# Kernel optimization log

Measured on AMD Instinct MI355X. Metric: run time of the kernel, lower is better.

Reference implementation:

```python
import jax, jax.numpy as jnp
import numpy as np

N = 12000   # num_node
D = 128     # hiddenSize
HID = 256   # hidden_channels
B = 512     # batch
L = 20      # citing history length
F = 400     # title_vec + journal_vec
FF = 512    # transformer dim_feedforward
NH = 4      # heads
STDV = float(1.0 / np.sqrt(D))


def _unif(k, shape):
    return jax.random.uniform(k, shape, jnp.float32, -STDV, STDV)


def setup_inputs():
    key = jax.random.key(0)
    ks = jax.random.split(key, 40)
    inp = {}
    inp['embedding'] = _unif(ks[0], (N, D))
    inp['f1_w'] = _unif(ks[1], (D, F)); inp['f1_b'] = _unif(ks[2], (D,))
    # two GNN modules, each a 2-layer GCN (assumed structure)
    inp['gcn0_w1'] = _unif(ks[3], (D, HID)); inp['gcn0_b1'] = _unif(ks[4], (HID,))
    inp['gcn0_w2'] = _unif(ks[5], (HID, D)); inp['gcn0_b2'] = _unif(ks[6], (D,))
    inp['gcn1_w1'] = _unif(ks[7], (D, HID)); inp['gcn1_b1'] = _unif(ks[8], (HID,))
    inp['gcn1_w2'] = _unif(ks[9], (HID, D)); inp['gcn1_b2'] = _unif(ks[10], (D,))
    # transformer encoder layer (post-norm, relu), reset_parameters makes ALL weights uniform
    inp['in_proj_w'] = _unif(ks[11], (3 * D, D)); inp['in_proj_b'] = _unif(ks[12], (3 * D,))
    inp['out_proj_w'] = _unif(ks[13], (D, D)); inp['out_proj_b'] = _unif(ks[14], (D,))
    inp['ln1_s'] = _unif(ks[15], (D,)); inp['ln1_b'] = _unif(ks[16], (D,))
    inp['ff1_w'] = _unif(ks[17], (FF, D)); inp['ff1_b'] = _unif(ks[18], (FF,))
    inp['ff2_w'] = _unif(ks[19], (D, FF)); inp['ff2_b'] = _unif(ks[20], (D,))
    inp['ln2_s'] = _unif(ks[21], (D,)); inp['ln2_b'] = _unif(ks[22], (D,))
    # forward inputs
    inp['adj_mat'] = jax.random.uniform(ks[23], (N, N), jnp.float32) * (2.0 / N)  # ~row-stochastic
    inp['node_feature'] = jax.random.normal(ks[24], (N, F), jnp.float32)
    inp['H_content'] = jax.random.normal(ks[25], (B, 10), jnp.float32)  # unused in forward
    inp['citing'] = jax.random.randint(ks[26], (B,), 0, N)
    inp['h_items'] = jax.random.randint(ks[27], (B,), 0, N)  # unused in forward
    inp['u_seqs'] = jax.random.randint(ks[28], (B, L), 0, N)
    inp['u_seqs_num'] = jax.random.randint(ks[29], (B,), 1, L)  # unused in forward
    return inp


def _layer_norm(x, s, b):
    m = x.mean(-1, keepdims=True)
    v = ((x - m) ** 2).mean(-1, keepdims=True)
    return (x - m) * jax.lax.rsqrt(v + 1e-5) * s + b


def reference(embedding, f1_w, f1_b,
              gcn0_w1, gcn0_b1, gcn0_w2, gcn0_b2,
              gcn1_w1, gcn1_b1, gcn1_w2, gcn1_b2,
              in_proj_w, in_proj_b, out_proj_w, out_proj_b,
              ln1_s, ln1_b, ff1_w, ff1_b, ff2_w, ff2_b, ln2_s, ln2_b,
              adj_mat, node_feature, H_content,
              citing, h_items, u_seqs, u_seqs_num):
    # embedding gate
    nf = node_feature @ f1_w.T + f1_b          # [N, D]
    x = embedding * nf                          # [N, D]
    # GCN stack: each GNN = relu((A x) W1 + b1) -> (A h) W2 + b2
    for (w1, b1, w2, b2) in ((gcn0_w1, gcn0_b1, gcn0_w2, gcn0_b2),
                             (gcn1_w1, gcn1_b1, gcn1_w2, gcn1_b2)):
        h = jax.nn.relu((adj_mat @ x) @ w1 + b1)
        x = (adj_mat @ h) @ w2 + b2
    item = x                                    # [N, D]
    seq = item[u_seqs]                          # [B, L, D]
    # torch TransformerEncoderLayer with batch_first=False: dim0 (B) is the
    # sequence axis, dim1 (L) is the batch axis (faithful to original code).
    qkv = seq @ in_proj_w.T + in_proj_b         # [B, L, 3D]
    q, k, v = jnp.split(qkv, 3, axis=-1)
    dh = D // NH
    q = q.reshape(B, L, NH, dh) * (1.0 / np.sqrt(dh))
    k = k.reshape(B, L, NH, dh)
    v = v.reshape(B, L, NH, dh)
    att = jax.nn.softmax(jnp.einsum('snhd,tnhd->nhst', q, k), axis=-1)  # attn over seq axis s,t=B
    o = jnp.einsum('nhst,tnhd->snhd', att, v).reshape(B, L, D)
    o = o @ out_proj_w.T + out_proj_b
    x1 = _layer_norm(seq + o, ln1_s, ln1_b)
    ff = jax.nn.relu(x1 @ ff1_w.T + ff1_b) @ ff2_w.T + ff2_b
    x2 = _layer_norm(x1 + ff, ln2_s, ln2_b)
    citing_vec = x2.mean(axis=1)                # mean over dim=1 (L), [B, D]
    citing_feats = nf[citing]                   # [B, D]
    citing_paper = jnp.concatenate([citing_vec, citing_feats], axis=1)  # [B, 2D]
    cited_paper = jnp.concatenate([item, nf], axis=1)                   # [N, 2D]
    scores = citing_paper @ cited_paper.T       # [B, N]
    return scores
```

## Files before the change

### kernel.cpp

```cpp
#include <hip/hip_runtime.h>
#include <hip/hip_bf16.h>

typedef __hip_bfloat16 bf;
typedef __attribute__((ext_vector_type(4))) float f32x4;
typedef __attribute__((ext_vector_type(8))) __bf16 bf16x8;
typedef __attribute__((ext_vector_type(8))) short short8;

#define NN 12000
#define DD 128
#define HIDC 256
#define BBATCH 512
#define LSEQ 20
#define FFEAT 400
#define FFDIM 512
#define KSLICE 2400

__device__ __forceinline__ float b2f(bf v) { return __bfloat162float(v); }
__device__ __forceinline__ bf f2b(float v) { return __float2bfloat16(v); }
__device__ __forceinline__ float us2f(unsigned short u) {
    return __uint_as_float(((unsigned int)u) << 16);
}
__device__ __forceinline__ unsigned short f2us(float f) {
    bf h = __float2bfloat16(f);
    return __builtin_bit_cast(unsigned short, h);
}

__device__ __forceinline__ void gload_lds16(const bf* g, bf* l) {
    __builtin_amdgcn_global_load_lds(
        (__attribute__((address_space(1))) void*)(g),
        (__attribute__((address_space(3))) void*)(l),
        16, 0, 0);
}

template<bool F32>
__device__ __forceinline__ short8 ld8(const void* p, long long idx) {
    if (F32) {
        const float* fp = (const float*)p + idx;
        f32x4 u0 = *(const f32x4*)fp;
        f32x4 u1 = *(const f32x4*)(fp + 4);
        short8 s;
        s[0] = (short)f2us(u0[0]); s[1] = (short)f2us(u0[1]);
        s[2] = (short)f2us(u0[2]); s[3] = (short)f2us(u0[3]);
        s[4] = (short)f2us(u1[0]); s[5] = (short)f2us(u1[1]);
        s[6] = (short)f2us(u1[2]); s[7] = (short)f2us(u1[3]);
        return s;
    } else {
        return *(const short8*)((const bf*)p + idx);
    }
}

template<bool F32>
__device__ __forceinline__ bf ldelem(const void* p, long long idx) {
    if (F32) return f2b(((const float*)p)[idx]);
    return ((const bf*)p)[idx];
}

__global__ __launch_bounds__(256) void adj_gemm(
    const bf* __restrict__ A,
    const bf* __restrict__ Bt,
    float* __restrict__ part)
{
    alignas(16) __shared__ bf As[128 * 32];
    alignas(16) __shared__ bf Bs[128 * 32];
    const int tid = threadIdx.x;
    const int lane = tid & 63;
    const int w = tid >> 6;
    const int z = blockIdx.y;
    const long long k0 = (long long)z * KSLICE;
    int m0 = blockIdx.x * 128;
    if (m0 > NN - 128) m0 = NN - 128;

    const int r0 = 16 * (2 * w)     + (lane >> 2);
    const int r1 = 16 * (2 * w + 1) + (lane >> 2);
    const int cp = lane & 3;
    const int cl0 = cp ^ ((r0 >> 1) & 3);
    const int cl1 = cp ^ ((r1 >> 1) & 3);
    const bf* ga0 = A + (long long)(m0 + r0) * NN + k0 + cl0 * 8;
    const bf* ga1 = A + (long long)(m0 + r1) * NN + k0 + cl1 * 8;
    const bf* gb0 = Bt + (long long)r0 * NN + k0 + cl0 * 8;
    const bf* gb1 = Bt + (long long)r1 * NN + k0 + cl1 * 8;
    bf* lA0 = &As[16 * (2 * w) * 32];
    bf* lA1 = &As[16 * (2 * w + 1) * 32];
    bf* lB0 = &Bs[16 * (2 * w) * 32];
    bf* lB1 = &Bs[16 * (2 * w + 1) * 32];

    const int wr = (w >> 1) * 64, wc = (w & 1) * 64;
    const int fr = lane & 15;
    const int cphys = (lane >> 4) ^ ((fr >> 1) & 3);
    f32x4 acc[4][4] = {};

    for (int ks = 0; ks < KSLICE; ks += 32) {
        gload_lds16(ga0, lA0);
        gload_lds16(ga1, lA1);
        gload_lds16(gb0, lB0);
        gload_lds16(gb1, lB1);
        ga0 += 32; ga1 += 32; gb0 += 32; gb1 += 32;
        __syncthreads();
        bf16x8 af[4], bfr[4];
        #pragma unroll
        for (int i = 0; i < 4; i++)
            af[i] = *(const bf16x8*)((const char*)As + (wr + i * 16 + fr) * 64 + cphys * 16);
        #pragma unroll
        for (int i = 0; i < 4; i++)
            bfr[i] = *(const bf16x8*)((const char*)Bs + (wc + i * 16 + fr) * 64 + cphys * 16);
        #pragma unroll
        for (int mi = 0; mi < 4; mi++)
            #pragma unroll
            for (int ni = 0; ni < 4; ni++)
                acc[mi][ni] = __builtin_amdgcn_mfma_f32_16x16x32_bf16(
                    af[mi], bfr[ni], acc[mi][ni], 0, 0, 0);
        __syncthreads();
    }

    float* C = part + (long long)z * ((long long)NN * 128);
    const int cr0 = (lane >> 4) * 4;
    const int cc = lane & 15;
    #pragma unroll
    for (int mi = 0; mi < 4; mi++) {
        #pragma unroll
        for (int ni = 0; ni < 4; ni++) {
            int col = wc + ni * 16 + cc;
            #pragma unroll
            for (int j = 0; j < 4; j++) {
                int row = m0 + wr + mi * 16 + cr0 + j;
                C[(long long)row * 128 + col] = acc[mi][ni][j];
            }
        }
    }
}

template<bool A_F32, bool B_F32, bool HAS_BIAS, bool RELU, bool OUT_F32, bool SIDE_A>
__global__ __launch_bounds__(256) void gemm128(
    const void* __restrict__ A, int lda, long long sA1, long long sA2,
    const void* __restrict__ Bm, int ldb, long long sB1, long long sB2,
    const float* __restrict__ bias,
    void* __restrict__ Cv, int ldc, long long sC1, long long sC2,
    int M, int N, int K, int tilesN, int zdiv, float alpha,
    bf* __restrict__ sideA)
{
    __shared__ bf As[128][40];
    __shared__ bf Bs[128][40];
    const int tid = threadIdx.x;
    const int z = blockIdx.y;
    const int zq = z / zdiv, zr = z - zq * zdiv;
    const char* Ap = (const char*)A;
    const char* Bp = (const char*)Bm;
    const long long offA = (long long)zq * sA1 + (long long)zr * sA2;
    const long long offB = (long long)zq * sB1 + (long long)zr * sB2;
    const long long offC = (long long)zq * sC1 + (long long)zr * sC2;
    const int tm = blockIdx.x / tilesN, tn = blockIdx.x - tm * tilesN;
    int m0 = tm * 128; if (m0 > M - 128) m0 = M - 128;
    const int n0 = tn * 128;
    const int lane = tid & 63;
    const int wv = tid >> 6;
    const int wr = (wv >> 1) * 64, wc = (wv & 1) * 64;
    const int fr = lane & 15;
    const int kq = (lane >> 4) * 8;
    const int sr = tid >> 2, scol = (tid & 3) * 8;
    f32x4 acc[4][4] = {};

    for (int k0 = 0; k0 < K; k0 += 32) {
        if (k0 + 32 <= K) {
            const long long ia0 = offA + (long long)(m0 + sr) * lda + k0 + scol;
            const long long ia1 = offA + (long long)(m0 + sr + 64) * lda + k0 + scol;
            short8 va0 = ld8<A_F32>(Ap, ia0);
            short8 va1 = ld8<A_F32>(Ap, ia1);
            short8 vb0 = {0,0,0,0,0,0,0,0}, vb1 = {0,0,0,0,0,0,0,0};
            if (n0 + sr < N)      vb0 = ld8<B_F32>(Bp, offB + (long long)(n0 + sr) * ldb + k0 + scol);
            if (n0 + sr + 64 < N) vb1 = ld8<B_F32>(Bp, offB + (long long)(n0 + sr + 64) * ldb + k0 + scol);
            if (SIDE_A) {
                *(short8*)&sideA[ia0] = va0;
                *(short8*)&sideA[ia1] = va1;
            }
            *(short8*)&As[sr][scol] = va0;
            *(short8*)&As[sr + 64][scol] = va1;
            *(short8*)&Bs[sr][scol] = vb0;
            *(short8*)&Bs[sr + 64][scol] = vb1;
        } else {
            bf zv = f2b(0.f);
            for (int i = tid; i < 128 * 32; i += 256) {
                int r = i >> 5, c = i & 31, gk = k0 + c;
                As[r][c] = (gk < K) ? ldelem<A_F32>(Ap, offA + (long long)(m0 + r) * lda + gk) : zv;
                Bs[r][c] = (gk < K && n0 + r < N) ? ldelem<B_F32>(Bp, offB + (long long)(n0 + r) * ldb + gk) : zv;
            }
        }
        __syncthreads();
        bf16x8 af[4], bfg[4];
        #pragma unroll
        for (int i = 0; i < 4; i++) af[i]  = *(const bf16x8*)&As[wr + i * 16 + fr][kq];
        #pragma unroll
        for (int i = 0; i < 4; i++) bfg[i] = *(const bf16x8*)&Bs[wc + i * 16 + fr][kq];
        #pragma unroll
        for (int mi = 0; mi < 4; mi++)
            #pragma unroll
            for (int ni = 0; ni < 4; ni++)
                acc[mi][ni] = __builtin_amdgcn_mfma_f32_16x16x32_bf16(
                    af[mi], bfg[ni], acc[mi][ni], 0, 0, 0);
        __syncthreads();
    }

    const int cr0 = (lane >> 4) * 4;
    const int cc = lane & 15;
    #pragma unroll
    for (int mi = 0; mi < 4; mi++) {
        #pragma unroll
        for (int ni = 0; ni < 4; ni++) {
            int col = n0 + wc + ni * 16 + cc;
            if (col >= N) continue;
            float bv = 0.f;
            if (HAS_BIAS) bv = bias[col];
            #pragma unroll
            for (int j = 0; j < 4; j++) {
                int row = m0 + wr + mi * 16 + cr0 + j;
                float v = acc[mi][ni][j] * alpha + bv;
                if (RELU) v = fmaxf(v, 0.f);
                if (OUT_F32) ((float*)Cv)[offC + (long long)row * ldc + col] = v;
                else ((bf*)Cv)[offC + (long long)row * ldc + col] = f2b(v);
            }
        }
    }
}

template<bool IN_F32>
__global__ __launch_bounds__(256) void transpose_k(
    const void* __restrict__ in, int ldin, long long sI1, long long sI2, int zdiv,
    const float* __restrict__ mulp, int ldmul,
    bf* __restrict__ outp, int ldout, long long sOut,
    int R, int C)
{
    __shared__ bf t[32][33];
    const int z = blockIdx.z;
    const int zq = z / zdiv, zr = z - zq * zdiv;
    const long long offI = (long long)zq * sI1 + (long long)zr * sI2;
    bf* op = outp + (long long)z * sOut;
    int r0 = blockIdx.x * 32, c0 = blockIdx.y * 32;
    int tx = threadIdx.x, ty = threadIdx.y;
    #pragma unroll
    for (int i = 0; i < 4; i++) {
        int r = r0 + ty + i * 8, c = c0 + tx;
        bf v = f2b(0.f);
        if (r < R && c < C) {
            v = ldelem<IN_F32>(in, offI + (long long)r * ldin + c);
            if (mulp) v = f2b(b2f(v) * mulp[(long long)r * ldmul + c]);
        }
        t[ty + i * 8][tx] = v;
    }
    __syncthreads();
    #pragma unroll
    for (int i = 0; i < 4; i++) {
        int c = c0 + ty + i * 8, r = r0 + tx;
        if (c < C && r < R) op[(long long)c * ldout + r] = t[tx][ty + i * 8];
    }
}

__global__ __launch_bounds__(256) void reduceK(
    const float* __restrict__ part, const float* __restrict__ bias,
    bf* __restrict__ outp, int total, int nz, long long zs)
{
    int i = blockIdx.x * 256 + threadIdx.x;
    if (i >= total) return;
    float s = 0.f;
    for (int zz = 0; zz < nz; zz++) s += part[(long long)zz * zs + i];
    if (bias) s += bias[i & 127];
    outp[i] = f2b(s);
}

__global__ __launch_bounds__(256) void gather_rows(
    const bf* __restrict__ src, const int* __restrict__ idx,
    bf* __restrict__ dst, int nrows)
{
    int t = blockIdx.x * 256 + threadIdx.x;
    int row = t >> 4, p = t & 15;
    if (row >= nrows) return;
    long long srow = idx[row];
    *(short8*)&dst[(long long)row * 128 + p * 8] =
        *(const short8*)&src[srow * 128 + p * 8];
}

__global__ __launch_bounds__(256) void softmax512(bf* __restrict__ S, int nrows)
{
    int gid = blockIdx.x * 256 + threadIdx.x;
    int wid = gid >> 6, lane = gid & 63;
    if (wid >= nrows) return;
    bf* row = S + (long long)wid * 512;
    short8 raw = *(const short8*)&row[lane * 8];
    float v[8];
    float mx = -3.0e38f;
    #pragma unroll
    for (int j = 0; j < 8; j++) {
        v[j] = us2f((unsigned short)raw[j]);
        mx = fmaxf(mx, v[j]);
    }
    #pragma unroll
    for (int off = 32; off; off >>= 1) mx = fmaxf(mx, __shfl_xor(mx, off, 64));
    float sum = 0.f;
    #pragma unroll
    for (int j = 0; j < 8; j++) { v[j] = __expf(v[j] - mx); sum += v[j]; }
    #pragma unroll
    for (int off = 32; off; off >>= 1) sum += __shfl_xor(sum, off, 64);
    float inv = 1.f / sum;
    short8 o;
    #pragma unroll
    for (int j = 0; j < 8; j++) o[j] = (short)f2us(v[j] * inv);
    *(short8*)&row[lane * 8] = o;
}

__global__ __launch_bounds__(256) void ln_rows(
    const bf* __restrict__ a, const bf* __restrict__ bres,
    const float* __restrict__ sc, const float* __restrict__ bi,
    bf* __restrict__ outp, int nrows)
{
    int gid = blockIdx.x * 256 + threadIdx.x;
    int wid = gid >> 6, lane = gid & 63;
    if (wid >= nrows) return;
    long long base = (long long)wid * 128;
    int i0 = lane * 2, i1 = lane * 2 + 1;
    float x0 = b2f(a[base + i0]) + b2f(bres[base + i0]);
    float x1 = b2f(a[base + i1]) + b2f(bres[base + i1]);
    float s = x0 + x1;
    #pragma unroll
    for (int off = 32; off; off >>= 1) s += __shfl_xor(s, off, 64);
    float mean = s * (1.f / 128.f);
    float d0 = x0 - mean, d1 = x1 - mean;
    float vv = d0 * d0 + d1 * d1;
    #pragma unroll
    for (int off = 32; off; off >>= 1) vv += __shfl_xor(vv, off, 64);
    float inv = rsqrtf(vv * (1.f / 128.f) + 1e-5f);
    outp[base + i0] = f2b(d0 * inv * sc[i0] + bi[i0]);
    outp[base + i1] = f2b(d1 * inv * sc[i1] + bi[i1]);
}

__global__ __launch_bounds__(256) void build_citing(
    const bf* __restrict__ x2, const bf* __restrict__ nf,
    const int* __restrict__ citing, bf* __restrict__ cp)
{
    int i = blockIdx.x * 256 + threadIdx.x;
    if (i >= BBATCH * 256) return;
    int b = i >> 8, d = i & 255;
    float v;
    if (d < 128) {
        float s = 0.f;
        for (int l = 0; l < LSEQ; l++)
            s += b2f(x2[((long long)b * LSEQ + l) * 128 + d]);
        v = s * (1.f / (float)LSEQ);
    } else {
        v = b2f(nf[(long long)citing[b] * 128 + (d - 128)]);
    }
    cp[i] = f2b(v);
}

__global__ __launch_bounds__(256) void build_cited(
    const bf* __restrict__ item, const bf* __restrict__ nf, bf* __restrict__ outp)
{
    int i = blockIdx.x * 256 + threadIdx.x;
    if (i >= NN * 256) return;
    int r = i >> 8, d = i & 255;
    outp[i] = (d < 128) ? item[(long long)r * 128 + d]
                        : nf[(long long)r * 128 + (d - 128)];
}

extern "C" void kernel_launch(void* const* d_in, const int* in_sizes, int n_in,
                              void* d_out, int out_size, void* d_ws, size_t ws_size,
                              hipStream_t stream)
{
    const float* emb  = (const float*)d_in[0];
    const float* f1w  = (const float*)d_in[1];
    const float* f1b  = (const float*)d_in[2];
    const float* g0w1 = (const float*)d_in[3];  const float* g0b1 = (const float*)d_in[4];
    const float* g0w2 = (const float*)d_in[5];  const float* g0b2 = (const float*)d_in[6];
    const float* g1w1 = (const float*)d_in[7];  const float* g1b1 = (const float*)d_in[8];
    const float* g1w2 = (const float*)d_in[9];  const float* g1b2 = (const float*)d_in[10];
    const float* ipw  = (const float*)d_in[11]; const float* ipb  = (const float*)d_in[12];
    const float* opw  = (const float*)d_in[13]; const float* opb  = (const float*)d_in[14];
    const float* ln1s = (const float*)d_in[15]; const float* ln1b = (const float*)d_in[16];
    const float* ff1w = (const float*)d_in[17]; const float* ff1b = (const float*)d_in[18];
    const float* ff2w = (const float*)d_in[19]; const float* ff2b = (const float*)d_in[20];
    const float* ln2s = (const float*)d_in[21]; const float* ln2b = (const float*)d_in[22];
    const float* adj  = (const float*)d_in[23];
    const float* nfe  = (const float*)d_in[24];
    const int* citing = (const int*)d_in[26];
    const int* useqs  = (const int*)d_in[28];
    float* outp = (float*)d_out;

    size_t off = 0;
    auto carve = [&](size_t bytes) -> char* {
        char* p = (char*)d_ws + off;
        off += (bytes + 255) & ~(size_t)255;
        return p;
    };
    bf* adjb = (bf*)carve((size_t)NN * NN * 2);
    bf* nf   = (bf*)carve((size_t)NN * DD * 2);
    bf* bufP = (bf*)carve((size_t)NN * DD * 2);
    bf* bufQ = (bf*)carve((size_t)NN * DD * 2);
    bf* BT   = (bf*)carve((size_t)NN * DD * 2);
    bf* Hbuf = (bf*)carve((size_t)NN * HIDC * 2);
    float* part = (float*)carve((size_t)5 * NN * DD * 4);
    bf* seq  = (bf*)carve((size_t)10240 * DD * 2);
    bf* qkv  = (bf*)carve((size_t)10240 * 384 * 2);
    bf* Sb   = (bf*)carve((size_t)80 * 512 * 512 * 2);
    bf* w10T = (bf*)carve((size_t)DD * HIDC * 2);
    bf* w20T = (bf*)carve((size_t)DD * HIDC * 2);
    bf* w11T = (bf*)carve((size_t)DD * HIDC * 2);
    bf* w21T = (bf*)carve((size_t)DD * HIDC * 2);
    bf* x1ln = (bf*)Hbuf;
    bf* cp   = (bf*)((char*)Hbuf + (size_t)10240 * DD * 2);
    char* pr = (char*)part;
    bf* VT   = (bf*)pr; pr += (size_t)80 * 32 * 512 * 2;
    bf* o_   = (bf*)pr; pr += (size_t)10240 * DD * 2;
    bf* o2   = (bf*)pr; pr += (size_t)10240 * DD * 2;
    bf* ffh  = (bf*)pr; pr += (size_t)10240 * FFDIM * 2;
    bf* ff2o = (bf*)pr; pr += (size_t)10240 * DD * 2;
    bf* x2   = (bf*)pr; pr += (size_t)10240 * DD * 2;
    bf* cited= (bf*)pr; pr += (size_t)NN * 256 * 2;

    dim3 tb(256), tt(32, 8);
    const long long NM = (long long)NN * DD;

    transpose_k<true><<<dim3(4, 8, 1), tt, 0, stream>>>(g0w1, HIDC, 0, 0, 1, nullptr, 0, w10T, DD, 0, DD, HIDC);
    transpose_k<true><<<dim3(8, 4, 1), tt, 0, stream>>>(g0w2, DD, 0, 0, 1, nullptr, 0, w20T, HIDC, 0, HIDC, DD);
    transpose_k<true><<<dim3(4, 8, 1), tt, 0, stream>>>(g1w1, HIDC, 0, 0, 1, nullptr, 0, w11T, DD, 0, DD, HIDC);
    transpose_k<true><<<dim3(8, 4, 1), tt, 0, stream>>>(g1w2, DD, 0, 0, 1, nullptr, 0, w21T, HIDC, 0, HIDC, DD);

    gemm128<true, true, true, false, false, false><<<dim3(94, 1), tb, 0, stream>>>(
        nfe, FFEAT, 0, 0, f1w, FFEAT, 0, 0, f1b,
        nf, DD, 0, 0, NN, DD, FFEAT, 1, 1, 1.f, nullptr);
    transpose_k<false><<<dim3(375, 4, 1), tt, 0, stream>>>(nf, DD, 0, 0, 1, emb, DD, BT, NN, 0, NN, DD);

    const float* biases2[2] = { g0b2, g1b2 };
    const float* biases1[2] = { g0b1, g1b1 };
    const bf* w1T[2] = { w10T, w11T };
    const bf* w2T[2] = { w20T, w21T };
    bf* xout[2] = { bufP, bufQ };

    for (int g = 0; g < 2; g++) {
        if (g == 0) {
            gemm128<true, false, false, false, true, true><<<dim3(94, 5), tb, 0, stream>>>(
                adj, NN, 2400, 0, BT, NN, 2400, 0, nullptr,
                part, DD, NM, 0, NN, DD, 2400, 1, 1, 1.f, adjb);
        } else {
            adj_gemm<<<dim3(94, 5), tb, 0, stream>>>(adjb, BT, part);
        }
        bf* tbuf = (g == 0) ? bufP : bufQ;
        reduceK<<<dim3((NM + 255) / 256), tb, 0, stream>>>(part, nullptr, tbuf, (int)NM, 5, NM);
        gemm128<false, false, true, true, false, false><<<dim3(188, 1), tb, 0, stream>>>(
            tbuf, DD, 0, 0, w1T[g], DD, 0, 0, biases1[g],
            Hbuf, HIDC, 0, 0, NN, HIDC, DD, 2, 1, 1.f, nullptr);
        bf* t2buf = (g == 0) ? bufQ : bufP;
        gemm128<false, false, false, false, false, false><<<dim3(94, 1), tb, 0, stream>>>(
            Hbuf, HIDC, 0, 0, w2T[g], HIDC, 0, 0, nullptr,
            t2buf, DD, 0, 0, NN, DD, HIDC, 1, 1, 1.f, nullptr);
        transpose_k<false><<<dim3(375, 4, 1), tt, 0, stream>>>(t2buf, DD, 0, 0, 1, nullptr, 0, BT, NN, 0, NN, DD);
        adj_gemm<<<dim3(94, 5), tb, 0, stream>>>(adjb, BT, part);
        reduceK<<<dim3((NM + 255) / 256), tb, 0, stream>>>(part, biases2[g], xout[g], (int)NM, 5, NM);
        if (g == 0) {
            transpose_k<false><<<dim3(375, 4, 1), tt, 0, stream>>>(bufP, DD, 0, 0, 1, nullptr, 0, BT, NN, 0, NN, DD);
        }
    }
    bf* item = bufQ;

    gather_rows<<<dim3(640), tb, 0, stream>>>(item, useqs, seq, 10240);
    gemm128<false, true, true, false, false, false><<<dim3(240, 1), tb, 0, stream>>>(
        seq, DD, 0, 0, ipw, DD, 0, 0, ipb,
        qkv, 384, 0, 0, 10240, 384, DD, 3, 1, 1.f, nullptr);
    transpose_k<false><<<dim3(16, 1, 80), tt, 0, stream>>>(
        qkv + 256, 7680, 384, 32, 4, nullptr, 0, VT, 512, 16384, 512, 32);
    gemm128<false, false, false, false, false, false><<<dim3(16, 80), tb, 0, stream>>>(
        qkv, 7680, 384, 32, qkv + 128, 7680, 384, 32, nullptr,
        Sb, 512, (long long)4 * 262144, 262144, 512, 512, 32, 4, 4, 0.17677669529663687f, nullptr);
    softmax512<<<dim3(10240), tb, 0, stream>>>(Sb, 80 * 512);
    gemm128<false, false, false, false, false, false><<<dim3(4, 80), tb, 0, stream>>>(
        Sb, 512, (long long)4 * 262144, 262144, VT, 512, (long long)4 * 16384, 16384, nullptr,
        o_, 2560, 128, 32, 512, 32, 512, 1, 4, 1.f, nullptr);
    gemm128<false, true, true, false, false, false><<<dim3(80, 1), tb, 0, stream>>>(
        o_, DD, 0, 0, opw, DD, 0, 0, opb,
        o2, DD, 0, 0, 10240, DD, DD, 1, 1, 1.f, nullptr);
    ln_rows<<<dim3(2560), tb, 0, stream>>>(seq, o2, ln1s, ln1b, x1ln, 10240);
    gemm128<false, true, true, true, false, false><<<dim3(320, 1), tb, 0, stream>>>(
        x1ln, DD, 0, 0, ff1w, DD, 0, 0, ff1b,
        ffh, FFDIM, 0, 0, 10240, FFDIM, DD, 4, 1, 1.f, nullptr);
    gemm128<false, true, true, false, false, false><<<dim3(80, 1), tb, 0, stream>>>(
        ffh, FFDIM, 0, 0, ff2w, FFDIM, 0, 0, ff2b,
        ff2o, DD, 0, 0, 10240, DD, FFDIM, 1, 1, 1.f, nullptr);
    ln_rows<<<dim3(2560), tb, 0, stream>>>(x1ln, ff2o, ln2s, ln2b, x2, 10240);
    build_citing<<<dim3(512), tb, 0, stream>>>(x2, nf, citing, cp);
    build_cited<<<dim3(12000), tb, 0, stream>>>(item, nf, cited);
    gemm128<false, false, false, false, true, false><<<dim3(376, 1), tb, 0, stream>>>(
        cp, 256, 0, 0, cited, 256, 0, 0, nullptr,
        outp, NN, 0, 0, BBATCH, NN, 256, 94, 1, 1.f, nullptr);
}
```

Before: 808.4 us.

## Double-buffer adjacency GEMM LDS tiles and halve M tile to raise block count

The adjacency GEMM kernel now prefetches the next K-step into a second LDS buffer while computing on the current one, which removes one barrier per iteration and overlaps global loads with MFMA work. The M tile shrinks from 128 to 64 rows, so the grid grows from 94x5 to 188x5 blocks (940 instead of 470) to fill more CUs on the MI355X. In exchange, each block re-reads the full 128-column B tile, which doubles B traffic per unit of output, and each warp does fewer MFMAs per LDS load.

```diff
diff --git a/kernel.cpp b/kernel.cpp
--- a/kernel.cpp
+++ b/kernel.cpp
@@ -55,68 +55,82 @@
     return ((const bf*)p)[idx];
 }
 
-__global__ __launch_bounds__(256) void adj_gemm(
+__global__ __launch_bounds__(256) void adj_gemm2(
     const bf* __restrict__ A,
     const bf* __restrict__ Bt,
     float* __restrict__ part)
 {
-    alignas(16) __shared__ bf As[128 * 32];
-    alignas(16) __shared__ bf Bs[128 * 32];
+    alignas(16) __shared__ bf As[2][64 * 32];
+    alignas(16) __shared__ bf Bs[2][128 * 32];
     const int tid = threadIdx.x;
     const int lane = tid & 63;
     const int w = tid >> 6;
     const int z = blockIdx.y;
     const long long k0 = (long long)z * KSLICE;
-    int m0 = blockIdx.x * 128;
-    if (m0 > NN - 128) m0 = NN - 128;
-
-    const int r0 = 16 * (2 * w)     + (lane >> 2);
-    const int r1 = 16 * (2 * w + 1) + (lane >> 2);
-    const int cp = lane & 3;
-    const int cl0 = cp ^ ((r0 >> 1) & 3);
-    const int cl1 = cp ^ ((r1 >> 1) & 3);
-    const bf* ga0 = A + (long long)(m0 + r0) * NN + k0 + cl0 * 8;
-    const bf* ga1 = A + (long long)(m0 + r1) * NN + k0 + cl1 * 8;
-    const bf* gb0 = Bt + (long long)r0 * NN + k0 + cl0 * 8;
-    const bf* gb1 = Bt + (long long)r1 * NN + k0 + cl1 * 8;
-    bf* lA0 = &As[16 * (2 * w) * 32];
-    bf* lA1 = &As[16 * (2 * w + 1) * 32];
-    bf* lB0 = &Bs[16 * (2 * w) * 32];
-    bf* lB1 = &Bs[16 * (2 * w + 1) * 32];
-
-    const int wr = (w >> 1) * 64, wc = (w & 1) * 64;
+    int m0 = blockIdx.x * 64;
+    if (m0 > NN - 64) m0 = NN - 64;
+
+    const int rA  = 16 * w + (lane >> 2);
+    const int rB0 = 32 * w + (lane >> 2);
+    const int rB1 = 32 * w + 16 + (lane >> 2);
+    const int cpn = lane & 3;
+    const int clA  = cpn ^ ((rA  >> 1) & 3);
+    const int clB0 = cpn ^ ((rB0 >> 1) & 3);
+    const int clB1 = cpn ^ ((rB1 >> 1) & 3);
+    const bf* gA  = A  + (long long)(m0 + rA) * NN + k0 + clA * 8;
+    const bf* gB0 = Bt + (long long)rB0 * NN + k0 + clB0 * 8;
+    const bf* gB1 = Bt + (long long)rB1 * NN + k0 + clB1 * 8;
+    const int loA  = 16 * w * 32;
+    const int loB0 = 32 * w * 32;
+    const int loB1 = (32 * w + 16) * 32;
+
+    const int wr = (w >> 1) * 32, wc = (w & 1) * 64;
     const int fr = lane & 15;
-    const int cphys = (lane >> 4) ^ ((fr >> 1) & 3);
-    f32x4 acc[4][4] = {};
-
-    for (int ks = 0; ks < KSLICE; ks += 32) {
-        gload_lds16(ga0, lA0);
-        gload_lds16(ga1, lA1);
-        gload_lds16(gb0, lB0);
-        gload_lds16(gb1, lB1);
-        ga0 += 32; ga1 += 32; gb0 += 32; gb1 += 32;
-        __syncthreads();
-        bf16x8 af[4], bfr[4];
-        #pragma unroll
-        for (int i = 0; i < 4; i++)
-            af[i] = *(const bf16x8*)((const char*)As + (wr + i * 16 + fr) * 64 + cphys * 16);
-        #pragma unroll
-        for (int i = 0; i < 4; i++)
-            bfr[i] = *(const bf16x8*)((const char*)Bs + (wc + i * 16 + fr) * 64 + cphys * 16);
-        #pragma unroll
-        for (int mi = 0; mi < 4; mi++)
+    const int kq = lane >> 4;
+    f32x4 acc[2][4] = {};
+
+    gload_lds16(gA,  &As[0][loA]);
+    gload_lds16(gB0, &Bs[0][loB0]);
+    gload_lds16(gB1, &Bs[0][loB1]);
+    __syncthreads();
+
+    int cur = 0;
+    #pragma unroll 1
+    for (int ks = 0; ks < KSLICE / 32; ks++) {
+        if (ks + 1 < KSLICE / 32) {
+            const int go = (ks + 1) * 32;
+            gload_lds16(gA + go,  &As[cur ^ 1][loA]);
+            gload_lds16(gB0 + go, &Bs[cur ^ 1][loB0]);
+            gload_lds16(gB1 + go, &Bs[cur ^ 1][loB1]);
+        }
+        const char* Ab = (const char*)&As[cur][0];
+        const char* Bb = (const char*)&Bs[cur][0];
+        bf16x8 af[2], bfr[4];
+        #pragma unroll
+        for (int i = 0; i < 2; i++) {
+            int row = wr + i * 16 + fr;
+            af[i] = *(const bf16x8*)(Ab + row * 64 + (kq ^ ((row >> 1) & 3)) * 16);
+        }
+        #pragma unroll
+        for (int i = 0; i < 4; i++) {
+            int row = wc + i * 16 + fr;
+            bfr[i] = *(const bf16x8*)(Bb + row * 64 + (kq ^ ((row >> 1) & 3)) * 16);
+        }
+        #pragma unroll
+        for (int mi = 0; mi < 2; mi++)
             #pragma unroll
             for (int ni = 0; ni < 4; ni++)
                 acc[mi][ni] = __builtin_amdgcn_mfma_f32_16x16x32_bf16(
                     af[mi], bfr[ni], acc[mi][ni], 0, 0, 0);
         __syncthreads();
+        cur ^= 1;
     }
 
     float* C = part + (long long)z * ((long long)NN * 128);
     const int cr0 = (lane >> 4) * 4;
     const int cc = lane & 15;
     #pragma unroll
-    for (int mi = 0; mi < 4; mi++) {
+    for (int mi = 0; mi < 2; mi++) {
         #pragma unroll
         for (int ni = 0; ni < 4; ni++) {
             int col = wc + ni * 16 + cc;
@@ -438,7 +452,7 @@
                 adj, NN, 2400, 0, BT, NN, 2400, 0, nullptr,
                 part, DD, NM, 0, NN, DD, 2400, 1, 1, 1.f, adjb);
         } else {
-            adj_gemm<<<dim3(94, 5), tb, 0, stream>>>(adjb, BT, part);
+            adj_gemm2<<<dim3(188, 5), tb, 0, stream>>>(adjb, BT, part);
         }
         bf* tbuf = (g == 0) ? bufP : bufQ;
         reduceK<<<dim3((NM + 255) / 256), tb, 0, stream>>>(part, nullptr, tbuf, (int)NM, 5, NM);
@@ -450,7 +464,7 @@
             Hbuf, HIDC, 0, 0, w2T[g], HIDC, 0, 0, nullptr,
             t2buf, DD, 0, 0, NN, DD, HIDC, 1, 1, 1.f, nullptr);
         transpose_k<false><<<dim3(375, 4, 1), tt, 0, stream>>>(t2buf, DD, 0, 0, 1, nullptr, 0, BT, NN, 0, NN, DD);
-        adj_gemm<<<dim3(94, 5), tb, 0, stream>>>(adjb, BT, part);
+        adj_gemm2<<<dim3(188, 5), tb, 0, stream>>>(adjb, BT, part);
         reduceK<<<dim3((NM + 255) / 256), tb, 0, stream>>>(part, biases2[g], xout[g], (int)NM, 5, NM);
         if (g == 0) {
             transpose_k<false><<<dim3(375, 4, 1), tt, 0, stream>>>(bufP, DD, 0, 0, 1, nullptr, 0, BT, NN, 0, NN, DD);
```

Result: slower. 898.6 us (+11.2%).
